# Kernel tuning notes

Measured on AMD Instinct MI355X. Metric: run time of the kernel, lower is better.

Reference implementation:

```python
import jax, jax.numpy as jnp
import numpy as np

N = 50000      # node_each_graph
K = 16         # fixed neighbor degree
D_IN = 128     # in_feats
D_H = 128      # n_hidden
C = 8          # n_classes
N_GATED = 3    # n_layers - 1
EPS = 1e-5     # LayerNorm eps
CLAMP = 1e-5   # entropy clamp


def _layernorm(x):
    # LayerNorm over the full node vector, elementwise_affine=False
    m = jnp.mean(x)
    v = jnp.mean((x - m) ** 2)
    return (x - m) / jnp.sqrt(v + EPS)


def setup_inputs() -> dict:
    key = jax.random.key(0)
    ks = jax.random.split(key, 8)
    feat = jax.random.normal(ks[0], (N, D_IN), jnp.float32)
    neighbors = jax.random.randint(ks[1], (N, K), 0, N)  # int neighbor ids
    s = 1.0 / np.sqrt(D_H)
    W_gcn = jax.random.uniform(ks[2], (D_IN, D_H), jnp.float32, -s, s)
    b_gcn = jax.random.uniform(ks[3], (D_H,), jnp.float32, -s, s)
    Wy = jax.random.normal(ks[4], (D_H, C), jnp.float32) * 0.05
    by = jnp.zeros((C,), jnp.float32)
    tau1 = jnp.zeros((1,), jnp.float32)  # global_tau_1 (shared_tau=True)
    tau2 = jnp.zeros((1,), jnp.float32)  # global_tau_2
    Wc = jax.random.normal(ks[5], (D_H * N, C), jnp.float32) * 1e-3
    bc = jnp.zeros((C,), jnp.float32)
    return {"feat": feat, "W_gcn": W_gcn, "b_gcn": b_gcn, "Wy": Wy,
            "by": by, "tau1": tau1, "tau2": tau2, "Wc": Wc, "bc": bc,
            "neighbors": neighbors}


def reference(feat, W_gcn, b_gcn, Wy, by, tau1, tau2, Wc, bc, neighbors):
    # Layer 0: GCNLayer (no activation, no dropout)
    h = feat @ W_gcn                      # [N, D_H]
    h = h[neighbors].sum(axis=1) + b_gcn  # neighbor-sum aggregation

    old_z = jnp.float32(1.0)
    for _ in range(N_GATED):
        # logits = softmax(weight_y(h))
        logits = jax.nn.softmax(h @ Wy + by, axis=1)          # [N, C]
        # adaptive_reduce_func (n_degree hard-coded to 1 in source)
        nb_logits = logits[neighbors]                          # [N, K, C]
        pred = jnp.argmax(nb_logits, axis=2)                   # [N, K]
        center = jnp.argmax(logits, axis=1)                    # [N]
        f1 = jnp.sum(pred == center[:, None], axis=1).astype(jnp.float32)
        # class histogram per node (== torch.unique loop when all classes occur)
        cnts = jax.nn.one_hot(pred, C, dtype=jnp.float32).sum(axis=1)  # [N, C]
        cnts = jnp.clip(cnts, CLAMP, None)
        f2 = -jnp.sum(cnts * jnp.log(cnts), axis=1)
        f1 = jax.lax.stop_gradient(f1)
        f2 = jax.lax.stop_gradient(f2)
        norm_f1 = _layernorm(f1)
        norm_f2 = _layernorm(f2)
        z = jax.nn.sigmoid(-(norm_f1 - tau1[0])) * jax.nn.sigmoid(-(norm_f2 - tau2[0]))
        gate = jnp.minimum(old_z, z)                           # [N]
        agg = h[neighbors].sum(axis=1)                         # [N, D_H]
        h = h + gate[:, None] * agg                            # activation=None
        old_z = z

    out = h.reshape(1, -1) @ Wc + bc                           # [1, C]
    return out
```

## Files before the change

### kernel.cpp

```cpp
#include <hip/hip_runtime.h>
#include <math.h>

#define NN 50000
#define DD 128
#define KK 16
#define CC 8
#define NCH 4
#define NB_AGG 1563

#define A_OFF    0u
#define B_OFF    (NN*DD*4u)
#define CENT_OFF (2u*NN*DD*4u)
#define Z0_OFF   (CENT_OFF + NN*4u)
#define Z1_OFF   (Z0_OFF + NN*4u)
#define F1_OFF   (Z1_OFF + NN*4u)
#define F2_OFF   (F1_OFF + NN*4u)
#define SU_OFF   (F2_OFF + NN*4u)
#define SD_OFF   (SU_OFF + 8u)
#define OACC_OFF (SD_OFF + 16u)

__global__ __launch_bounds__(256) void k_gemm(const float* __restrict__ feat,
    const float* __restrict__ W, float* __restrict__ A, double* __restrict__ oacc)
{
    __shared__ __align__(16) float sW[DD*DD];
    __shared__ float sF[64][DD+1];
    const int t = threadIdx.x;
    const int base = blockIdx.x * 64;
    if (blockIdx.x == 0 && t < CC) oacc[t] = 0.0;

    const float4* W4 = (const float4*)W;
    float4* sW4 = (float4*)sW;
    #pragma unroll
    for (int i = 0; i < 16; ++i) sW4[t + i*256] = W4[t + i*256];

    const float4* F4 = (const float4*)feat;
    #pragma unroll
    for (int e = t; e < 64*32; e += 256) {
        int row = e >> 5, q = e & 31;
        float4 v = make_float4(0.f,0.f,0.f,0.f);
        if (base + row < NN) v = F4[(size_t)(base + row)*32 + q];
        sF[row][q*4+0] = v.x; sF[row][q*4+1] = v.y;
        sF[row][q*4+2] = v.z; sF[row][q*4+3] = v.w;
    }
    __syncthreads();

    const int cg = t & 15;
    const int ng = t >> 4;
    const int cb = cg * 8;
    float acc[4][8];
    #pragma unroll
    for (int j=0;j<4;++j)
        #pragma unroll
        for (int c=0;c<8;++c) acc[j][c]=0.f;

    #pragma unroll 4
    for (int d = 0; d < DD; ++d) {
        float4 wa = *(const float4*)&sW[d*DD + cb];
        float4 wb = *(const float4*)&sW[d*DD + cb + 4];
        #pragma unroll
        for (int j=0;j<4;++j) {
            float f = sF[ng*4+j][d];
            acc[j][0] += f*wa.x; acc[j][1] += f*wa.y;
            acc[j][2] += f*wa.z; acc[j][3] += f*wa.w;
            acc[j][4] += f*wb.x; acc[j][5] += f*wb.y;
            acc[j][6] += f*wb.z; acc[j][7] += f*wb.w;
        }
    }
    const int ch = cb >> 5;
    const int co = cb & 31;
    #pragma unroll
    for (int j=0;j<4;++j) {
        int node = base + ng*4 + j;
        if (node < NN) {
            float4* dst = (float4*)&A[((size_t)ch*NN + node)*32 + co];
            dst[0] = make_float4(acc[j][0],acc[j][1],acc[j][2],acc[j][3]);
            dst[1] = make_float4(acc[j][4],acc[j][5],acc[j][6],acc[j][7]);
        }
    }
}

__global__ __launch_bounds__(256) void k_agg0(const float4* __restrict__ A4,
    const int* __restrict__ nb, const float* __restrict__ bg,
    float4* __restrict__ H4, float* __restrict__ zold)
{
    const int t = threadIdx.x;
    const int c = blockIdx.x / NB_AGG;
    const int nbase = (blockIdx.x % NB_AGG) * 32;
    __shared__ int sIdx[32*KK];
    if (t < 128) {
        if (nbase + (t >> 2) < NN)
            ((int4*)sIdx)[t] = ((const int4*)(nb + (size_t)nbase*KK))[t];
    }
    __syncthreads();
    const int nl = t >> 3;
    const int q  = t & 7;
    const int node = nbase + nl;
    if (node >= NN) return;
    float4 acc = ((const float4*)bg)[c*8 + q];
    #pragma unroll
    for (int k=0;k<KK;++k) {
        int idx = sIdx[nl*KK + k];
        float4 v = A4[((size_t)c*NN + idx)*8 + q];
        acc.x += v.x; acc.y += v.y; acc.z += v.z; acc.w += v.w;
    }
    H4[((size_t)c*NN + node)*8 + q] = acc;
    if (c == 0 && q == 0) zold[node] = 1.0f;
}

__global__ __launch_bounds__(256) void k_center(const float* __restrict__ H,
    const float* __restrict__ Wy, const float* __restrict__ by,
    int* __restrict__ center, unsigned* __restrict__ su, double* __restrict__ sd)
{
    const int t = threadIdx.x;
    if (blockIdx.x == 0) {
        if (t < 2) su[t] = 0u;
        if (t >= 2 && t < 4) sd[t-2] = 0.0;
    }
    __shared__ float sH[64][DD+1];
    __shared__ __align__(16) float sWy[DD*CC];
    __shared__ float sby[CC];
    const int base = blockIdx.x * 64;
    const float4* H4 = (const float4*)H;
    #pragma unroll
    for (int e = t; e < 64*32; e += 256) {
        int row = e >> 5, q = e & 31;
        int ch = q >> 3, q8 = q & 7;
        float4 v = make_float4(0.f,0.f,0.f,0.f);
        if (base + row < NN) v = H4[((size_t)ch*NN + base+row)*8 + q8];
        sH[row][q*4+0] = v.x; sH[row][q*4+1] = v.y;
        sH[row][q*4+2] = v.z; sH[row][q*4+3] = v.w;
    }
    ((float4*)sWy)[t] = ((const float4*)Wy)[t & 255];
    if (t < CC) sby[t] = by[t];
    __syncthreads();

    const int nl = t >> 2;
    const int c0 = (t & 3) * 2;
    float a0 = 0.f, a1 = 0.f;
    #pragma unroll 8
    for (int d = 0; d < DD; ++d) {
        float f = sH[nl][d];
        a0 += f * sWy[d*CC + c0];
        a1 += f * sWy[d*CC + c0 + 1];
    }
    a0 += sby[c0]; a1 += sby[c0+1];
    float bv = a0; int bi = c0;
    if (a1 > bv) { bv = a1; bi = c0 + 1; }
    #pragma unroll
    for (int off = 1; off < 4; off <<= 1) {
        float ov = __shfl_xor(bv, off, 64);
        int   oi = __shfl_xor(bi, off, 64);
        if (ov > bv || (ov == bv && oi < bi)) { bv = ov; bi = oi; }
    }
    const int node = base + nl;
    if ((t & 3) == 0 && node < NN) center[node] = bi;
}

__global__ __launch_bounds__(256) void k_stats(const int* __restrict__ center,
    const int* __restrict__ nb, float* __restrict__ f1o, float* __restrict__ f2o,
    unsigned* __restrict__ su, double* __restrict__ sd)
{
    const int t = threadIdx.x;
    const int i = blockIdx.x*256 + t;
    unsigned uf1 = 0, uf1sq = 0;
    double df2 = 0.0, df2sq = 0.0;
    if (i < NN) {
        const int ci = center[i];
        const int* nbi = nb + i*KK;
        unsigned long long cnt = 0ull;
        #pragma unroll
        for (int k=0;k<KK;++k) {
            int p = center[nbi[k]];
            cnt += 1ull << (p*8);
        }
        unsigned c1 = (unsigned)((cnt >> (ci*8)) & 0xFFull);
        float f2 = 0.f;
        #pragma unroll
        for (int c=0;c<CC;++c) {
            float fc = (float)((cnt >> (c*8)) & 0xFFull);
            fc = fmaxf(fc, 1e-5f);
            f2 -= fc * logf(fc);
        }
        f1o[i] = (float)c1;
        f2o[i] = f2;
        uf1 = c1; uf1sq = c1*c1;
        df2 = (double)f2; df2sq = df2*df2;
    }
    #pragma unroll
    for (int off = 32; off > 0; off >>= 1) {
        uf1   += __shfl_down(uf1,   off, 64);
        uf1sq += __shfl_down(uf1sq, off, 64);
        df2   += __shfl_down(df2,   off, 64);
        df2sq += __shfl_down(df2sq, off, 64);
    }
    __shared__ unsigned r1[4], r1s[4];
    __shared__ double   r2[4], r2s[4];
    const int wid = t >> 6, lane = t & 63;
    if (lane == 0) { r1[wid]=uf1; r1s[wid]=uf1sq; r2[wid]=df2; r2s[wid]=df2sq; }
    __syncthreads();
    if (t == 0) {
        atomicAdd(&su[0], r1[0]+r1[1]+r1[2]+r1[3]);
        atomicAdd(&su[1], r1s[0]+r1s[1]+r1s[2]+r1s[3]);
        atomicAdd(&sd[0], r2[0]+r2[1]+r2[2]+r2[3]);
        atomicAdd(&sd[1], r2s[0]+r2s[1]+r2s[2]+r2s[3]);
    }
}

__global__ __launch_bounds__(256) void k_update(const float4* __restrict__ Hin4,
    float4* __restrict__ Hout4, const int* __restrict__ nb,
    const float* __restrict__ f1, const float* __restrict__ f2,
    const float* __restrict__ zr, float* __restrict__ zw,
    const unsigned* __restrict__ su, const double* __restrict__ sd,
    const float* __restrict__ tau1, const float* __restrict__ tau2)
{
    const int t = threadIdx.x;
    const int c = blockIdx.x / NB_AGG;
    const int nbase = (blockIdx.x % NB_AGG) * 32;
    __shared__ int sIdx[32*KK];
    if (t < 128) {
        if (nbase + (t >> 2) < NN)
            ((int4*)sIdx)[t] = ((const int4*)(nb + (size_t)nbase*KK))[t];
    }
    __syncthreads();
    const int nl = t >> 3;
    const int q  = t & 7;
    const int node = nbase + nl;
    if (node >= NN) return;

    const double invN = 1.0 / (double)NN;
    double mu1  = (double)su[0] * invN;
    double var1 = (double)su[1] * invN - mu1*mu1;
    double is1  = 1.0 / sqrt(var1 + 1e-5);
    double mu2  = sd[0] * invN;
    double var2 = sd[1] * invN - mu2*mu2;
    double is2  = 1.0 / sqrt(var2 + 1e-5);
    float nf1 = (float)(((double)f1[node] - mu1) * is1);
    float nf2 = (float)(((double)f2[node] - mu2) * is2);
    float z = (1.0f/(1.0f + expf(nf1 - tau1[0]))) * (1.0f/(1.0f + expf(nf2 - tau2[0])));
    float gate = fminf(zr[node], z);
    if (c == 0 && q == 0) zw[node] = z;

    float4 acc = make_float4(0.f,0.f,0.f,0.f);
    #pragma unroll
    for (int k=0;k<KK;++k) {
        int idx = sIdx[nl*KK + k];
        float4 v = Hin4[((size_t)c*NN + idx)*8 + q];
        acc.x += v.x; acc.y += v.y; acc.z += v.z; acc.w += v.w;
    }
    float4 h = Hin4[((size_t)c*NN + node)*8 + q];
    h.x += gate*acc.x; h.y += gate*acc.y; h.z += gate*acc.z; h.w += gate*acc.w;
    Hout4[((size_t)c*NN + node)*8 + q] = h;
}

__global__ __launch_bounds__(256) void k_final(const float* __restrict__ H,
    const float4* __restrict__ Wc4, double* __restrict__ oacc)
{
    const int t = threadIdx.x;
    float a[8];
    #pragma unroll
    for (int c=0;c<8;++c) a[c]=0.f;
    const int R = NN*DD;
    for (int r = blockIdx.x*256 + t; r < R; r += gridDim.x*256) {
        int node = r >> 7, d = r & 127;
        float h = H[(((d>>5)*NN + node) << 5) + (d & 31)];
        float4 wa = Wc4[(size_t)r*2], wb = Wc4[(size_t)r*2 + 1];
        a[0]+=h*wa.x; a[1]+=h*wa.y; a[2]+=h*wa.z; a[3]+=h*wa.w;
        a[4]+=h*wb.x; a[5]+=h*wb.y; a[6]+=h*wb.z; a[7]+=h*wb.w;
    }
    #pragma unroll
    for (int off = 32; off > 0; off >>= 1)
        #pragma unroll
        for (int c=0;c<8;++c) a[c] += __shfl_down(a[c], off, 64);
    __shared__ double sred[4][8];
    const int wid = t >> 6, lane = t & 63;
    if (lane == 0) {
        #pragma unroll
        for (int c=0;c<8;++c) sred[wid][c] = (double)a[c];
    }
    __syncthreads();
    if (t < 8) {
        double s = sred[0][t]+sred[1][t]+sred[2][t]+sred[3][t];
        atomicAdd(&oacc[t], s);
    }
}

__global__ void k_fin(const double* __restrict__ oacc, const float* __restrict__ bc,
                      float* __restrict__ out)
{
    const int t = threadIdx.x;
    if (t < CC) out[t] = (float)(oacc[t] + (double)bc[t]);
}

extern "C" void kernel_launch(void* const* d_in, const int* in_sizes, int n_in,
                              void* d_out, int out_size, void* d_ws, size_t ws_size,
                              hipStream_t stream)
{
    const float* feat = (const float*)d_in[0];
    const float* Wg   = (const float*)d_in[1];
    const float* bg   = (const float*)d_in[2];
    const float* Wy   = (const float*)d_in[3];
    const float* by   = (const float*)d_in[4];
    const float* tau1 = (const float*)d_in[5];
    const float* tau2 = (const float*)d_in[6];
    const float* Wc   = (const float*)d_in[7];
    const float* bc   = (const float*)d_in[8];
    const int*   nb   = (const int*)d_in[9];

    char* ws = (char*)d_ws;
    float*    A      = (float*)(ws + A_OFF);
    float*    B      = (float*)(ws + B_OFF);
    int*      center = (int*)(ws + CENT_OFF);
    float*    z0     = (float*)(ws + Z0_OFF);
    float*    z1     = (float*)(ws + Z1_OFF);
    float*    f1     = (float*)(ws + F1_OFF);
    float*    f2     = (float*)(ws + F2_OFF);
    unsigned* su     = (unsigned*)(ws + SU_OFF);
    double*   sd     = (double*)(ws + SD_OFF);
    double*   oacc   = (double*)(ws + OACC_OFF);

    k_gemm<<<(NN + 63)/64, 256, 0, stream>>>(feat, Wg, A, oacc);
    k_agg0<<<NCH*NB_AGG, 256, 0, stream>>>((const float4*)A, nb, bg, (float4*)B, z0);

    float* hcur = B; float* hnext = A;
    float* zcur = z0; float* znext = z1;
    for (int it = 0; it < 3; ++it) {
        k_center<<<(NN + 63)/64, 256, 0, stream>>>(hcur, Wy, by, center, su, sd);
        k_stats<<<(NN + 255)/256, 256, 0, stream>>>(center, nb, f1, f2, su, sd);
        k_update<<<NCH*NB_AGG, 256, 0, stream>>>((const float4*)hcur, (float4*)hnext,
                                                 nb, f1, f2, zcur, znext, su, sd, tau1, tau2);
        float* tmp = hcur; hcur = hnext; hnext = tmp;
        tmp = zcur; zcur = znext; znext = tmp;
    }
    k_final<<<2048, 256, 0, stream>>>(hcur, (const float4*)Wc, oacc);
    k_fin<<<1, 64, 0, stream>>>(oacc, bc, (float*)d_out);
}
```

Measured before the change: 591.5 us.

## Split hidden features into 8 chunks of 16 and fuse final bias kernel

Changes the chunked node-feature layout from 4 chunks of 32 floats to 8 chunks of 16 floats. Each gather in the aggregation and update kernels now fetches 64 bytes per neighbor row, so a chunk of 50000 rows (3.2 MB) is more likely to stay cache-resident while blocks gather across 64 nodes. The index tile is padded to avoid LDS bank conflicts. The separate k_fin launch is folded into k_final using a last-block ticket counter, which removes one kernel launch at the cost of a threadfence and an atomic.

```diff
diff --git a/kernel.cpp b/kernel.cpp
--- a/kernel.cpp
+++ b/kernel.cpp
@@ -5,8 +5,8 @@
 #define DD 128
 #define KK 16
 #define CC 8
-#define NCH 4
-#define NB_AGG 1563
+#define NCH 8
+#define NB8 782
 
 #define A_OFF    0u
 #define B_OFF    (NN*DD*4u)
@@ -18,15 +18,20 @@
 #define SU_OFF   (F2_OFF + NN*4u)
 #define SD_OFF   (SU_OFF + 8u)
 #define OACC_OFF (SD_OFF + 16u)
+#define TICK_OFF (OACC_OFF + 64u)
 
 __global__ __launch_bounds__(256) void k_gemm(const float* __restrict__ feat,
-    const float* __restrict__ W, float* __restrict__ A, double* __restrict__ oacc)
+    const float* __restrict__ W, float* __restrict__ A, double* __restrict__ oacc,
+    unsigned* __restrict__ tick)
 {
     __shared__ __align__(16) float sW[DD*DD];
     __shared__ float sF[64][DD+1];
     const int t = threadIdx.x;
     const int base = blockIdx.x * 64;
-    if (blockIdx.x == 0 && t < CC) oacc[t] = 0.0;
+    if (blockIdx.x == 0) {
+        if (t < CC) oacc[t] = 0.0;
+        if (t == CC) *tick = 0u;
+    }
 
     const float4* W4 = (const float4*)W;
     float4* sW4 = (float4*)sW;
@@ -66,13 +71,13 @@
             acc[j][6] += f*wb.z; acc[j][7] += f*wb.w;
         }
     }
-    const int ch = cb >> 5;
-    const int co = cb & 31;
+    const int ch = cb >> 4;
+    const int co = cb & 15;
     #pragma unroll
     for (int j=0;j<4;++j) {
         int node = base + ng*4 + j;
         if (node < NN) {
-            float4* dst = (float4*)&A[((size_t)ch*NN + node)*32 + co];
+            float4* dst = (float4*)&A[((size_t)ch*NN + node)*16 + co];
             dst[0] = make_float4(acc[j][0],acc[j][1],acc[j][2],acc[j][3]);
             dst[1] = make_float4(acc[j][4],acc[j][5],acc[j][6],acc[j][7]);
         }
@@ -84,26 +89,30 @@
     float4* __restrict__ H4, float* __restrict__ zold)
 {
     const int t = threadIdx.x;
-    const int c = blockIdx.x / NB_AGG;
-    const int nbase = (blockIdx.x % NB_AGG) * 32;
-    __shared__ int sIdx[32*KK];
-    if (t < 128) {
-        if (nbase + (t >> 2) < NN)
-            ((int4*)sIdx)[t] = ((const int4*)(nb + (size_t)nbase*KK))[t];
-    }
-    __syncthreads();
-    const int nl = t >> 3;
-    const int q  = t & 7;
+    const int c = blockIdx.x / NB8;
+    const int nbase = (blockIdx.x % NB8) * 64;
+    __shared__ int sIdx[64*17];
+    {
+        int nl = t >> 2, k4 = (t & 3) * 4;
+        if (nbase + nl < NN) {
+            int4 v = ((const int4*)(nb + (size_t)nbase*KK))[t];
+            sIdx[nl*17 + k4 + 0] = v.x; sIdx[nl*17 + k4 + 1] = v.y;
+            sIdx[nl*17 + k4 + 2] = v.z; sIdx[nl*17 + k4 + 3] = v.w;
+        }
+    }
+    __syncthreads();
+    const int nl = t >> 2;
+    const int q  = t & 3;
     const int node = nbase + nl;
     if (node >= NN) return;
-    float4 acc = ((const float4*)bg)[c*8 + q];
+    float4 acc = ((const float4*)bg)[c*4 + q];
     #pragma unroll
     for (int k=0;k<KK;++k) {
-        int idx = sIdx[nl*KK + k];
-        float4 v = A4[((size_t)c*NN + idx)*8 + q];
+        int idx = sIdx[nl*17 + k];
+        float4 v = A4[((size_t)c*NN + idx)*4 + q];
         acc.x += v.x; acc.y += v.y; acc.z += v.z; acc.w += v.w;
     }
-    H4[((size_t)c*NN + node)*8 + q] = acc;
+    H4[((size_t)c*NN + node)*4 + q] = acc;
     if (c == 0 && q == 0) zold[node] = 1.0f;
 }
 
@@ -124,9 +133,9 @@
     #pragma unroll
     for (int e = t; e < 64*32; e += 256) {
         int row = e >> 5, q = e & 31;
-        int ch = q >> 3, q8 = q & 7;
+        int ch = q >> 2, q4 = q & 3;
         float4 v = make_float4(0.f,0.f,0.f,0.f);
-        if (base + row < NN) v = H4[((size_t)ch*NN + base+row)*8 + q8];
+        if (base + row < NN) v = H4[((size_t)ch*NN + base+row)*4 + q4];
         sH[row][q*4+0] = v.x; sH[row][q*4+1] = v.y;
         sH[row][q*4+2] = v.z; sH[row][q*4+3] = v.w;
     }
@@ -214,16 +223,20 @@
     const float* __restrict__ tau1, const float* __restrict__ tau2)
 {
     const int t = threadIdx.x;
-    const int c = blockIdx.x / NB_AGG;
-    const int nbase = (blockIdx.x % NB_AGG) * 32;
-    __shared__ int sIdx[32*KK];
-    if (t < 128) {
-        if (nbase + (t >> 2) < NN)
-            ((int4*)sIdx)[t] = ((const int4*)(nb + (size_t)nbase*KK))[t];
-    }
-    __syncthreads();
-    const int nl = t >> 3;
-    const int q  = t & 7;
+    const int c = blockIdx.x / NB8;
+    const int nbase = (blockIdx.x % NB8) * 64;
+    __shared__ int sIdx[64*17];
+    {
+        int nl = t >> 2, k4 = (t & 3) * 4;
+        if (nbase + nl < NN) {
+            int4 v = ((const int4*)(nb + (size_t)nbase*KK))[t];
+            sIdx[nl*17 + k4 + 0] = v.x; sIdx[nl*17 + k4 + 1] = v.y;
+            sIdx[nl*17 + k4 + 2] = v.z; sIdx[nl*17 + k4 + 3] = v.w;
+        }
+    }
+    __syncthreads();
+    const int nl = t >> 2;
+    const int q  = t & 3;
     const int node = nbase + nl;
     if (node >= NN) return;
 
@@ -243,17 +256,19 @@
     float4 acc = make_float4(0.f,0.f,0.f,0.f);
     #pragma unroll
     for (int k=0;k<KK;++k) {
-        int idx = sIdx[nl*KK + k];
-        float4 v = Hin4[((size_t)c*NN + idx)*8 + q];
+        int idx = sIdx[nl*17 + k];
+        float4 v = Hin4[((size_t)c*NN + idx)*4 + q];
         acc.x += v.x; acc.y += v.y; acc.z += v.z; acc.w += v.w;
     }
-    float4 h = Hin4[((size_t)c*NN + node)*8 + q];
+    float4 h = Hin4[((size_t)c*NN + node)*4 + q];
     h.x += gate*acc.x; h.y += gate*acc.y; h.z += gate*acc.z; h.w += gate*acc.w;
-    Hout4[((size_t)c*NN + node)*8 + q] = h;
+    Hout4[((size_t)c*NN + node)*4 + q] = h;
 }
 
 __global__ __launch_bounds__(256) void k_final(const float* __restrict__ H,
-    const float4* __restrict__ Wc4, double* __restrict__ oacc)
+    const float4* __restrict__ Wc4, double* __restrict__ oacc,
+    unsigned* __restrict__ tick, const float* __restrict__ bc,
+    float* __restrict__ out)
 {
     const int t = threadIdx.x;
     float a[8];
@@ -262,7 +277,7 @@
     const int R = NN*DD;
     for (int r = blockIdx.x*256 + t; r < R; r += gridDim.x*256) {
         int node = r >> 7, d = r & 127;
-        float h = H[(((d>>5)*NN + node) << 5) + (d & 31)];
+        float h = H[(((d>>4)*NN + node) << 4) + (d & 15)];
         float4 wa = Wc4[(size_t)r*2], wb = Wc4[(size_t)r*2 + 1];
         a[0]+=h*wa.x; a[1]+=h*wa.y; a[2]+=h*wa.z; a[3]+=h*wa.w;
         a[4]+=h*wb.x; a[5]+=h*wb.y; a[6]+=h*wb.z; a[7]+=h*wb.w;
@@ -272,6 +287,7 @@
         #pragma unroll
         for (int c=0;c<8;++c) a[c] += __shfl_down(a[c], off, 64);
     __shared__ double sred[4][8];
+    __shared__ int last;
     const int wid = t >> 6, lane = t & 63;
     if (lane == 0) {
         #pragma unroll
@@ -282,13 +298,16 @@
         double s = sred[0][t]+sred[1][t]+sred[2][t]+sred[3][t];
         atomicAdd(&oacc[t], s);
     }
-}
-
-__global__ void k_fin(const double* __restrict__ oacc, const float* __restrict__ bc,
-                      float* __restrict__ out)
-{
-    const int t = threadIdx.x;
-    if (t < CC) out[t] = (float)(oacc[t] + (double)bc[t]);
+    __threadfence();
+    if (t == 0) {
+        unsigned rank = atomicAdd(tick, 1u);
+        last = (rank == (unsigned)(gridDim.x - 1)) ? 1 : 0;
+    }
+    __syncthreads();
+    if (last && t < CC) {
+        double v = atomicAdd(&oacc[t], 0.0);
+        out[t] = (float)(v + (double)bc[t]);
+    }
 }
 
 extern "C" void kernel_launch(void* const* d_in, const int* in_sizes, int n_in,
@@ -317,20 +336,20 @@
     unsigned* su     = (unsigned*)(ws + SU_OFF);
     double*   sd     = (double*)(ws + SD_OFF);
     double*   oacc   = (double*)(ws + OACC_OFF);
-
-    k_gemm<<<(NN + 63)/64, 256, 0, stream>>>(feat, Wg, A, oacc);
-    k_agg0<<<NCH*NB_AGG, 256, 0, stream>>>((const float4*)A, nb, bg, (float4*)B, z0);
+    unsigned* tick   = (unsigned*)(ws + TICK_OFF);
+
+    k_gemm<<<(NN + 63)/64, 256, 0, stream>>>(feat, Wg, A, oacc, tick);
+    k_agg0<<<NCH*NB8, 256, 0, stream>>>((const float4*)A, nb, bg, (float4*)B, z0);
 
     float* hcur = B; float* hnext = A;
     float* zcur = z0; float* znext = z1;
     for (int it = 0; it < 3; ++it) {
         k_center<<<(NN + 63)/64, 256, 0, stream>>>(hcur, Wy, by, center, su, sd);
         k_stats<<<(NN + 255)/256, 256, 0, stream>>>(center, nb, f1, f2, su, sd);
-        k_update<<<NCH*NB_AGG, 256, 0, stream>>>((const float4*)hcur, (float4*)hnext,
-                                                 nb, f1, f2, zcur, znext, su, sd, tau1, tau2);
+        k_update<<<NCH*NB8, 256, 0, stream>>>((const float4*)hcur, (float4*)hnext,
+                                              nb, f1, f2, zcur, znext, su, sd, tau1, tau2);
         float* tmp = hcur; hcur = hnext; hnext = tmp;
         tmp = zcur; zcur = znext; znext = tmp;
     }
-    k_final<<<2048, 256, 0, stream>>>(hcur, (const float4*)Wc, oacc);
-    k_fin<<<1, 64, 0, stream>>>(oacc, bc, (float*)d_out);
-}
+    k_final<<<2048, 256, 0, stream>>>(hcur, (const float4*)Wc, oacc, tick, bc, (float*)d_out);
+}
```

Measured after the change: 892.8 us. 51.0% more time.
